# Kernel tuning notes

Measured on AMD Instinct MI355X. Metric: run time of the kernel, lower is better.

The kernel has to match this reference:

```python
import jax, jax.numpy as jnp
import numpy as np

B, N, D_IN, H1, H2, L, SEM_H = 256, 128, 1024, 512, 256, 64, 32


def _topo_sort(adj_np):
    # Faithful replica of the source DFS 'topological sort' (treats row entries as neighbors,
    # appends node after visiting them, then reverses). Runs on concrete numpy at setup time.
    n = adj_np.shape[0]
    visited = [False] * n
    order = []
    def dfs(u):
        visited[u] = True
        for v in np.nonzero(adj_np[u])[0]:
            if not visited[v]:
                dfs(v)
        order.append(u)
    for u in range(n):
        if not visited[u]:
            dfs(u)
    return np.array(order[::-1], dtype=np.int32)


def setup_inputs() -> dict:
    key = jax.random.key(0)
    ks = jax.random.split(key, 32)
    def w(k, shape, fan_in):
        return jax.random.normal(k, shape, jnp.float32) / np.float32(np.sqrt(fan_in))
    inp = {
        'x': jax.random.normal(ks[0], (B, N, D_IN), jnp.float32),
        'eps': jax.random.normal(ks[1], (B, N, L), jnp.float32),
        'adj_logits': jax.random.normal(ks[2], (N, N), jnp.float32),
        # encoder: D_IN -> H1 -> H2
        'enc_W1': w(ks[3], (H1, D_IN), D_IN), 'enc_b1': jnp.zeros((H1,), jnp.float32),
        'enc_W2': w(ks[4], (H2, H1), H1),     'enc_b2': jnp.zeros((H2,), jnp.float32),
        'mu_W': w(ks[5], (L, H2), H2),        'mu_b': jnp.zeros((L,), jnp.float32),
        'lv_W': w(ks[6], (L, H2), H2),        'lv_b': jnp.zeros((L,), jnp.float32),
        # decoder: L -> H2 -> H1 -> D_IN (reversed(hidden_dims), final Linear(hidden_dims[0], D_IN))
        'dec_W1': w(ks[7], (H2, L), L),       'dec_b1': jnp.zeros((H2,), jnp.float32),
        'dec_W2': w(ks[8], (H1, H2), H2),     'dec_b2': jnp.zeros((H1,), jnp.float32),
        'dec_W3': w(ks[9], (D_IN, H1), H1),   'dec_b3': jnp.zeros((D_IN,), jnp.float32),
        # per-node SEM MLPs, stacked: Linear(2L, 32) -> ReLU -> Linear(32, L)
        'sem_W1': w(ks[10], (N, SEM_H, 2 * L), 2 * L), 'sem_b1': jnp.zeros((N, SEM_H), jnp.float32),
        'sem_W2': w(ks[11], (N, L, SEM_H), SEM_H),     'sem_b2': jnp.zeros((N, L), jnp.float32),
    }
    # deterministic eval-mode adjacency -> concrete topo order
    mask = 1.0 - np.eye(N, dtype=np.float32)
    adj_np = (np.asarray(inp['adj_logits']) * mask) > 0
    inp['topo_order'] = jnp.asarray(_topo_sort(adj_np))
    return inp


def reference(x, eps, adj_logits, enc_W1, enc_b1, enc_W2, enc_b2, mu_W, mu_b, lv_W, lv_b,
              dec_W1, dec_b1, dec_W2, dec_b2, dec_W3, dec_b3, sem_W1, sem_b1, sem_W2, sem_b2,
              topo_order):
    f32 = x.dtype
    # --- adjacency (eval mode: hard threshold of masked logits) ---
    mask = 1.0 - jnp.eye(N, dtype=f32)
    adj = ((adj_logits * mask) > 0).astype(f32)  # [N, N], row i = parents of node i
    # --- encode ---
    h = jax.nn.relu(jnp.einsum('bnd,hd->bnh', x, enc_W1) + enc_b1)
    h = jax.nn.relu(jnp.einsum('bnd,hd->bnh', h, enc_W2) + enc_b2)
    mu = jnp.einsum('bnd,ld->bnl', h, mu_W) + mu_b
    logvar = jnp.einsum('bnd,ld->bnl', h, lv_W) + lv_b
    # --- reparameterize ---
    z = mu + eps * jnp.exp(0.5 * logvar)  # [B, N, L]
    # --- SEM: sequential scan over topological order ---
    def step(tz, node):
        adj_row = adj[node]                              # [N]
        cnt = jnp.maximum(adj_row.sum(), 1.0)
        agg = jnp.einsum('n,bnl->bl', adj_row, tz) / cnt  # mean over parents
        feat = jnp.concatenate([z[:, node], agg], axis=-1)  # [B, 2L]
        hh = jax.nn.relu(feat @ sem_W1[node].T + sem_b1[node])
        out = hh @ sem_W2[node].T + sem_b2[node]          # [B, L]
        return tz.at[:, node].set(out), None
    tz0 = jnp.zeros_like(z)
    z_t, _ = jax.lax.scan(step, tz0, topo_order)
    # --- decode ---
    d = jax.nn.relu(jnp.einsum('bnl,hl->bnh', z_t, dec_W1) + dec_b1)
    d = jax.nn.relu(jnp.einsum('bnl,hl->bnh', d, dec_W2) + dec_b2)
    recon_x = jnp.einsum('bnl,hl->bnh', d, dec_W3) + dec_b3
    # --- KL ---
    kl_div = -0.5 * jnp.sum(1.0 + logvar - mu * mu - jnp.exp(logvar))
    return recon_x, mu, logvar, adj, kl_div
```

## Files before the change

kernel.cpp:

```cpp
#include <hip/hip_runtime.h>
#include <cstdint>
#include <cstddef>

typedef unsigned short u16;
typedef __attribute__((ext_vector_type(8))) short short8;
typedef __attribute__((ext_vector_type(4))) float f32x4;

__device__ __forceinline__ u16 f2b(float f) {
  union { float f; uint32_t u; } v; v.f = f;
  uint32_t u = v.u;
  uint32_t r = (u + 0x7FFFu + ((u >> 16) & 1u)) >> 16;
  return (u16)r;
}

__device__ __forceinline__ void gload_lds16(const void* g, void* l) {
  __builtin_amdgcn_global_load_lds(
      (const __attribute__((address_space(1))) void*)g,
      (__attribute__((address_space(3))) void*)l, 16, 0, 0);
}
__device__ __forceinline__ void gload_lds4(const void* g, void* l) {
  __builtin_amdgcn_global_load_lds(
      (const __attribute__((address_space(1))) void*)g,
      (__attribute__((address_space(3))) void*)l, 4, 0, 0);
}

__global__ void prep_adj(const float* __restrict__ logits, const int* __restrict__ topo,
                         float* __restrict__ adj_out, int* __restrict__ parlist,
                         int* __restrict__ ecnt, float* __restrict__ rcnt,
                         const float* __restrict__ mu_b, const float* __restrict__ lv_b,
                         float* __restrict__ mbias) {
  __shared__ int pos[128];
  int i = threadIdx.x;
  pos[topo[i]] = i;
  __syncthreads();
  int mypos = pos[i];
  int c_all = 0, c_eff = 0;
  for (int j = 0; j < 128; ++j) {
    float v = (i != j && logits[i * 128 + j] > 0.0f) ? 1.0f : 0.0f;
    adj_out[i * 128 + j] = v;
    if (v != 0.0f) {
      c_all++;
      if (pos[j] < mypos) parlist[i * 128 + c_eff++] = j;
    }
  }
  while (c_eff & 15) parlist[i * 128 + c_eff++] = 128;
  ecnt[i] = c_eff;
  rcnt[i] = 1.0f / fmaxf((float)c_all, 1.0f);
  mbias[i] = (i < 64) ? mu_b[i] : lv_b[i - 64];
}

__global__ void prep_semT(const float* __restrict__ W1, const float* __restrict__ W2,
                          const float* __restrict__ b1, const float* __restrict__ b2,
                          float* __restrict__ W1T, float* __restrict__ W2T,
                          float* __restrict__ biasP) {
  int node = blockIdx.x, t = threadIdx.x;
  const float* w1 = W1 + node * 4096;
  float* o1 = W1T + node * 4096;
  for (int e = t; e < 4096; e += 256) { int j = e >> 7, k = e & 127; o1[k * 32 + j] = w1[e]; }
  const float* w2 = W2 + node * 2048;
  float* o2 = W2T + node * 2048;
  for (int e = t; e < 2048; e += 256) { int l = e >> 5, k = e & 31; o2[k * 64 + l] = w2[e]; }
  if (t < 128) {
    float v = 0.0f;
    if (t < 32) v = b1[node * 32 + t];
    else if (t < 96) v = b2[node * 64 + (t - 32)];
    biasP[node * 128 + t] = v;
  }
}

__global__ __launch_bounds__(256)
void cvt_weights(const float* __restrict__ e1, const float* __restrict__ e2,
                 const float* __restrict__ muw, const float* __restrict__ lvw,
                 const float* __restrict__ d1, const float* __restrict__ d2,
                 const float* __restrict__ d3, u16* __restrict__ dst) {
  int i = blockIdx.x * 256 + threadIdx.x;
  int stride = gridDim.x * 256;
  for (; i < 1359872; i += stride) {
    float v;
    if      (i < 524288) v = e1[i];
    else if (i < 655360) v = e2[i - 524288];
    else if (i < 671744) v = muw[i - 655360];
    else if (i < 688128) v = lvw[i - 671744];
    else if (i < 704512) v = d1[i - 688128];
    else if (i < 835584) v = d2[i - 704512];
    else                 v = d3[i - 835584];
    dst[i] = f2b(v);
  }
}

__global__ __launch_bounds__(256)
void cvt_f32_bf16(const float* __restrict__ src, u16* __restrict__ dst, size_t n4) {
  size_t i = (size_t)blockIdx.x * blockDim.x + threadIdx.x;
  size_t stride = (size_t)gridDim.x * blockDim.x;
  for (; i < n4; i += stride) {
    float4 v = ((const float4*)src)[i];
    ushort4 o;
    o.x = f2b(v.x); o.y = f2b(v.y); o.z = f2b(v.z); o.w = f2b(v.w);
    ((ushort4*)dst)[i] = o;
  }
}

template <int OUT_MODE, int RELU>
__global__ __launch_bounds__(256)
void gemm_bt(const u16* __restrict__ A, const u16* __restrict__ W,
             const float* __restrict__ bias, void* __restrict__ Cout,
             int M, int Ncols, int K, int gx) {
  __shared__ __align__(16) u16 As[128 * 64];
  __shared__ __align__(16) u16 Bs[128 * 64];
  const int tid = threadIdx.x;
  const int bid = blockIdx.x;
  const int xcd = bid & 7, w = bid >> 3;
  const int gy8 = (int)(gridDim.x >> 3) / gx;
  const int tile_n = w % gx;
  const int tile_m = xcd * gy8 + w / gx;
  const int wid = tid >> 6, lane = tid & 63;
  const int wm = (wid >> 1) * 64, wn = (wid & 1) * 64;
  const int lr = lane & 15, lg = lane >> 4;
  f32x4 acc[4][4] = {};
  const size_t arow0 = (size_t)tile_m * 128;
  const size_t brow0 = (size_t)tile_n * 128;

  for (int kt = 0; kt < K; kt += 64) {
#pragma unroll
    for (int is = 0; is < 4; ++is) {
      int e = is * 2048 + tid * 8;
      int r = e >> 6, c = e & 63;
      gload_lds16(A + (arow0 + r) * K + kt + c, &As[e]);
      gload_lds16(W + (brow0 + r) * K + kt + c, &Bs[e]);
    }
    __syncthreads();
#pragma unroll
    for (int kk = 0; kk < 64; kk += 32) {
      short8 av[4], bv[4];
#pragma unroll
      for (int m = 0; m < 4; ++m)
        av[m] = *(const short8*)&As[(wm + m * 16 + lr) * 64 + kk + lg * 8];
#pragma unroll
      for (int n = 0; n < 4; ++n)
        bv[n] = *(const short8*)&Bs[(wn + n * 16 + lr) * 64 + kk + lg * 8];
#pragma unroll
      for (int m = 0; m < 4; ++m)
#pragma unroll
        for (int n = 0; n < 4; ++n)
          acc[m][n] = __builtin_amdgcn_mfma_f32_16x16x32_bf16(av[m], bv[n], acc[m][n], 0, 0, 0);
    }
    __syncthreads();
  }
#pragma unroll
  for (int n = 0; n < 4; ++n) {
    int col = (int)brow0 + wn + n * 16 + lr;
    float bval = bias[col];
#pragma unroll
    for (int m = 0; m < 4; ++m) {
#pragma unroll
      for (int r = 0; r < 4; ++r) {
        int row = (int)arow0 + wm + m * 16 + lg * 4 + r;
        float v = acc[m][n][r] + bval;
        if (RELU) v = fmaxf(v, 0.0f);
        if (OUT_MODE == 1) ((u16*)Cout)[(size_t)row * Ncols + col] = f2b(v);
        else if (OUT_MODE == 0) ((float*)Cout)[(size_t)row * Ncols + col] = v;
        else {
          float* muo = (float*)Cout;
          float* lvo = muo + 2097152;
          if (col < 64) muo[(size_t)row * 64 + col] = v;
          else          lvo[(size_t)row * 64 + (col - 64)] = v;
        }
      }
    }
  }
}

__global__ __launch_bounds__(256)
void reparam_kernel(const float* __restrict__ mo, const float* __restrict__ lo,
                    const float* __restrict__ eps,
                    float* __restrict__ z, float* __restrict__ klpart) {
  int gid = blockIdx.x * 256 + threadIdx.x;
  float mu = mo[gid];
  float lv = lo[gid];
  float e = eps[gid];
  z[gid] = mu + e * expf(0.5f * lv);
  float kt = 1.0f + lv - mu * mu - expf(lv);
  for (int o = 32; o > 0; o >>= 1) kt += __shfl_down(kt, o);
  __shared__ float red[4];
  int lane = threadIdx.x & 63, w = threadIdx.x >> 6;
  if (lane == 0) red[w] = kt;
  __syncthreads();
  if (threadIdx.x == 0) klpart[blockIdx.x] = red[0] + red[1] + red[2] + red[3];
}

__global__ void kl_final(const float* __restrict__ klpart, float* __restrict__ out) {
  __shared__ float red[256];
  float s = 0.0f;
  for (int i = threadIdx.x; i < 8192; i += 256) s += klpart[i];
  red[threadIdx.x] = s;
  __syncthreads();
  for (int st = 128; st > 0; st >>= 1) {
    if (threadIdx.x < st) red[threadIdx.x] += red[threadIdx.x + st];
    __syncthreads();
  }
  if (threadIdx.x == 0) out[0] = -0.5f * red[0];
}

__device__ __forceinline__ void sem_pref(int wid, int lane, int nd, int bi, int b,
    const float* __restrict__ W1Tg, const float* __restrict__ W2Tg,
    const float* __restrict__ biasPg, const int* __restrict__ parlist,
    const float* __restrict__ z,
    float (*w1s)[4096], float (*w2s)[2048], int (*pls)[128],
    float (*zrs)[64], float (*bis)[128]) {
  const float* w1g = W1Tg + (size_t)nd * 4096 + wid * 1024 + lane * 4;
  float* w1d = &w1s[bi][wid * 1024 + lane * 4];
#pragma unroll
  for (int q = 0; q < 4; ++q) gload_lds16(w1g + q * 256, w1d + q * 256);
  if (wid >= 2) {
    int h = wid - 2;
    const float* w2g = W2Tg + (size_t)nd * 2048 + h * 1024 + lane * 4;
    float* w2d = &w2s[bi][h * 1024 + lane * 4];
#pragma unroll
    for (int q = 0; q < 4; ++q) gload_lds16(w2g + q * 256, w2d + q * 256);
  } else if (wid == 0) {
    gload_lds4(parlist + nd * 128 + lane, &pls[bi][lane]);
    gload_lds4(parlist + nd * 128 + 64 + lane, &pls[bi][64 + lane]);
  } else {
    gload_lds4(z + ((size_t)b * 128 + nd) * 64 + lane, &zrs[bi][lane]);
    gload_lds4(biasPg + nd * 128 + lane, &bis[bi][lane]);
    gload_lds4(biasPg + nd * 128 + 64 + lane, &bis[bi][64 + lane]);
  }
}

__global__ __launch_bounds__(256)
void sem_scan4(const float* __restrict__ z, u16* __restrict__ ztb,
               const float* __restrict__ W1Tg, const float* __restrict__ W2Tg,
               const float* __restrict__ biasPg,
               const int* __restrict__ parlist, const int* __restrict__ ecnt,
               const float* __restrict__ rcnt, const int* __restrict__ topo) {
  const int b = blockIdx.x, t = threadIdx.x;
  const int lane = t & 63, wid = t >> 6;
  __shared__ __align__(16) float tz[129 * 64];
  __shared__ __align__(16) float w1s[2][4096];
  __shared__ __align__(16) float w2s[2][2048];
  __shared__ __align__(16) int   pls[2][128];
  __shared__ __align__(16) float zrs[2][64];
  __shared__ __align__(16) float bis[2][128];
  __shared__ float feat[128];
  __shared__ float aggP[256];
  __shared__ float part1[128];
  __shared__ float part2[256];
  __shared__ float hhs[32];
  __shared__ int topoS[128];
  __shared__ int ecS[128];
  __shared__ float rcS[128];

  for (int i = t; i < 129 * 64; i += 256) tz[i] = 0.0f;
  if (t < 128) { topoS[t] = topo[t]; ecS[t] = ecnt[t]; rcS[t] = rcnt[t]; }
  __syncthreads();

  sem_pref(wid, lane, topoS[0], 0, b, W1Tg, W2Tg, biasPg, parlist, z,
           w1s, w2s, pls, zrs, bis);

  for (int s = 0; s < 128; ++s) {
    const int cur = s & 1;
    const int node = topoS[s];
    asm volatile("s_waitcnt vmcnt(0)" ::: "memory");
    __syncthreads();
    if (s + 1 < 128)
      sem_pref(wid, lane, topoS[s + 1], cur ^ 1, b, W1Tg, W2Tg, biasPg, parlist, z,
               w1s, w2s, pls, zrs, bis);

    const int pc = ecS[node];
    const int* pl = pls[cur];
    float ap = 0.0f;
    for (int i = wid * 16; i < pc; i += 64) {
      int4 p0 = *(const int4*)&pl[i];
      int4 p1 = *(const int4*)&pl[i + 4];
      int4 p2 = *(const int4*)&pl[i + 8];
      int4 p3 = *(const int4*)&pl[i + 12];
      ap += tz[p0.x * 64 + lane]; ap += tz[p0.y * 64 + lane];
      ap += tz[p0.z * 64 + lane]; ap += tz[p0.w * 64 + lane];
      ap += tz[p1.x * 64 + lane]; ap += tz[p1.y * 64 + lane];
      ap += tz[p1.z * 64 + lane]; ap += tz[p1.w * 64 + lane];
      ap += tz[p2.x * 64 + lane]; ap += tz[p2.y * 64 + lane];
      ap += tz[p2.z * 64 + lane]; ap += tz[p2.w * 64 + lane];
      ap += tz[p3.x * 64 + lane]; ap += tz[p3.y * 64 + lane];
      ap += tz[p3.z * 64 + lane]; ap += tz[p3.w * 64 + lane];
    }
    aggP[wid * 64 + lane] = ap;
    __syncthreads();
    if (t < 64) {
      float agg = (aggP[t] + aggP[64 + t] + aggP[128 + t] + aggP[192 + t]) * rcS[node];
      feat[t] = zrs[cur][t];
      feat[64 + t] = agg;
    }
    __syncthreads();

    {
      const int j = t & 31, sub = t >> 5;
      const float* w1 = &w1s[cur][sub * 512];
      float a = 0.0f;
#pragma unroll
      for (int kk = 0; kk < 16; ++kk)
        a = fmaf(w1[kk * 32 + j], feat[sub * 16 + kk], a);
      a += __shfl_xor(a, 32);
      if (lane < 32) part1[wid * 32 + j] = a;
    }
    __syncthreads();
    if (t < 32) {
      float hv = part1[t] + part1[32 + t] + part1[64 + t] + part1[96 + t] + bis[cur][t];
      hhs[t] = fmaxf(hv, 0.0f);
    }
    __syncthreads();

    {
      const float* w2 = &w2s[cur][wid * 512];
      float o = 0.0f;
#pragma unroll
      for (int kk = 0; kk < 8; ++kk)
        o = fmaf(w2[kk * 64 + lane], hhs[wid * 8 + kk], o);
      part2[wid * 64 + lane] = o;
    }
    __syncthreads();
    if (t < 64) {
      float ov = part2[t] + part2[64 + t] + part2[128 + t] + part2[192 + t] + bis[cur][32 + t];
      tz[node * 64 + t] = ov;
      ztb[((size_t)b * 128 + node) * 64 + t] = f2b(ov);
    }
  }
}

extern "C" void kernel_launch(void* const* d_in, const int* in_sizes, int n_in,
                              void* d_out, int out_size, void* d_ws, size_t ws_size,
                              hipStream_t stream) {
  const float* x          = (const float*)d_in[0];
  const float* eps        = (const float*)d_in[1];
  const float* adj_logits = (const float*)d_in[2];
  const float* enc_W1     = (const float*)d_in[3];
  const float* enc_b1     = (const float*)d_in[4];
  const float* enc_W2     = (const float*)d_in[5];
  const float* enc_b2     = (const float*)d_in[6];
  const float* mu_W       = (const float*)d_in[7];
  const float* mu_b       = (const float*)d_in[8];
  const float* lv_W       = (const float*)d_in[9];
  const float* lv_b       = (const float*)d_in[10];
  const float* dec_W1     = (const float*)d_in[11];
  const float* dec_b1     = (const float*)d_in[12];
  const float* dec_W2     = (const float*)d_in[13];
  const float* dec_b2     = (const float*)d_in[14];
  const float* dec_W3     = (const float*)d_in[15];
  const float* dec_b3     = (const float*)d_in[16];
  const float* sem_W1     = (const float*)d_in[17];
  const float* sem_b1     = (const float*)d_in[18];
  const float* sem_W2     = (const float*)d_in[19];
  const float* sem_b2     = (const float*)d_in[20];
  const int*   topo       = (const int*)d_in[21];

  float* out       = (float*)d_out;
  float* out_recon = out;
  float* out_mu    = out + 33554432;
  float* out_lv    = out + 35651584;
  float* out_adj   = out + 37748736;
  float* out_kl    = out + 37765120;

  char* ws = (char*)d_ws;
  u16*   xb      = (u16*)(ws + 0);
  u16*   d2b     = (u16*)(ws + 0);
  u16*   h1b     = (u16*)(ws + 67108864);
  u16*   d1b     = h1b;
  u16*   h2b     = (u16*)(ws + 100663296);
  float* zbuf    = (float*)(ws + 117440512);
  u16*   ztb     = (u16*)(ws + 125829120);
  u16*   wb      = (u16*)(ws + 130023424);
  float* W1T     = (float*)(ws + 132743168);
  float* W2T     = (float*)(ws + 134840320);
  float* biasP   = (float*)(ws + 135888896);
  int*   parlist = (int*)(ws + 135954432);
  int*   ecnt    = (int*)(ws + 136019968);
  float* rcnt    = (float*)(ws + 136020480);
  float* mbias   = (float*)(ws + 136020992);
  float* klp     = (float*)(ws + 136021504);

  u16* wE1 = wb;
  u16* wE2 = wb + 524288;
  u16* wML = wb + 655360;
  u16* wD1 = wb + 688128;
  u16* wD2 = wb + 704512;
  u16* wD3 = wb + 835584;

  prep_adj<<<1, 128, 0, stream>>>(adj_logits, topo, out_adj, parlist, ecnt, rcnt, mu_b, lv_b, mbias);
  prep_semT<<<128, 256, 0, stream>>>(sem_W1, sem_W2, sem_b1, sem_b2, W1T, W2T, biasP);
  cvt_weights<<<512, 256, 0, stream>>>(enc_W1, enc_W2, mu_W, lv_W, dec_W1, dec_W2, dec_W3, wb);
  cvt_f32_bf16<<<4096, 256, 0, stream>>>(x, xb, 8388608);

  dim3 blk(256);
  gemm_bt<1, 1><<<dim3(4 * 256), blk, 0, stream>>>(xb,  wE1, enc_b1, h1b,    32768, 512, 1024, 4);
  gemm_bt<1, 1><<<dim3(2 * 256), blk, 0, stream>>>(h1b, wE2, enc_b2, h2b,    32768, 256, 512, 2);
  gemm_bt<2, 0><<<dim3(1 * 256), blk, 0, stream>>>(h2b, wML, mbias,  out_mu, 32768, 128, 256, 1);

  reparam_kernel<<<8192, 256, 0, stream>>>(out_mu, out_lv, eps, zbuf, klp);
  kl_final<<<1, 256, 0, stream>>>(klp, out_kl);

  sem_scan4<<<256, 256, 0, stream>>>(zbuf, ztb, W1T, W2T, biasP, parlist, ecnt, rcnt, topo);

  gemm_bt<1, 1><<<dim3(2 * 256), blk, 0, stream>>>(ztb, wD1, dec_b1, d1b,       32768, 256, 64, 2);
  gemm_bt<1, 1><<<dim3(4 * 256), blk, 0, stream>>>(d1b, wD2, dec_b2, d2b,       32768, 512, 256, 4);
  gemm_bt<0, 0><<<dim3(8 * 256), blk, 0, stream>>>(d2b, wD3, dec_b3, out_recon, 32768, 1024, 512, 8);
}
```

Before: 715.1 us.

## Parallelize adjacency prep, swizzle SEM weights, cut scan barriers, vectorize reparam

prep_adj now runs one block per node and builds each parent list with ballot/popcount instead of a single-block serial loop. The SEM W1 weights are stored with an XOR swizzle, and the per-step matvecs are restructured to reduce with shuffles, which removes two barriers and the partial-sum buffers per scan step. The scan also waits on fewer outstanding loads for some waves, and reparam uses float4 loads with a quarter as many blocks. The aim is to shorten the latency-bound sequential scan; the risk is the changed vmcnt wait and the shuffle reduction indexing.

```diff
diff --git a/kernel.cpp b/kernel.cpp
--- a/kernel.cpp
+++ b/kernel.cpp
@@ -24,42 +24,58 @@
       (__attribute__((address_space(3))) void*)l, 4, 0, 0);
 }
 
-__global__ void prep_adj(const float* __restrict__ logits, const int* __restrict__ topo,
-                         float* __restrict__ adj_out, int* __restrict__ parlist,
-                         int* __restrict__ ecnt, float* __restrict__ rcnt,
-                         const float* __restrict__ mu_b, const float* __restrict__ lv_b,
-                         float* __restrict__ mbias) {
-  __shared__ int pos[128];
-  int i = threadIdx.x;
-  pos[topo[i]] = i;
+__global__ __launch_bounds__(64)
+void prep_adj(const float* __restrict__ logits, const int* __restrict__ topo,
+              float* __restrict__ adj_out, int* __restrict__ parlist,
+              int* __restrict__ ecnt, float* __restrict__ rcnt,
+              const float* __restrict__ mu_b, const float* __restrict__ lv_b,
+              float* __restrict__ mbias) {
+  __shared__ int pos_s[128];
+  const int i = blockIdx.x, lane = threadIdx.x;
+  pos_s[topo[lane]] = lane;
+  pos_s[topo[64 + lane]] = 64 + lane;
   __syncthreads();
-  int mypos = pos[i];
-  int c_all = 0, c_eff = 0;
-  for (int j = 0; j < 128; ++j) {
-    float v = (i != j && logits[i * 128 + j] > 0.0f) ? 1.0f : 0.0f;
-    adj_out[i * 128 + j] = v;
-    if (v != 0.0f) {
-      c_all++;
-      if (pos[j] < mypos) parlist[i * 128 + c_eff++] = j;
-    }
-  }
-  while (c_eff & 15) parlist[i * 128 + c_eff++] = 128;
-  ecnt[i] = c_eff;
-  rcnt[i] = 1.0f / fmaxf((float)c_all, 1.0f);
-  mbias[i] = (i < 64) ? mu_b[i] : lv_b[i - 64];
-}
-
-__global__ void prep_semT(const float* __restrict__ W1, const float* __restrict__ W2,
+  const int myp = pos_s[i];
+  bool edge0 = (i != lane) && (logits[i * 128 + lane] > 0.0f);
+  bool edge1 = (i != 64 + lane) && (logits[i * 128 + 64 + lane] > 0.0f);
+  adj_out[i * 128 + lane] = edge0 ? 1.0f : 0.0f;
+  adj_out[i * 128 + 64 + lane] = edge1 ? 1.0f : 0.0f;
+  bool par0 = edge0 && (pos_s[lane] < myp);
+  bool par1 = edge1 && (pos_s[64 + lane] < myp);
+  uint64_t m0 = __ballot(par0);
+  uint64_t m1 = __ballot(par1);
+  uint64_t below = (lane == 0) ? 0ull : ((~0ull) >> (64 - lane));
+  int c0 = __popcll(m0);
+  int c_eff = c0 + __popcll(m1);
+  if (par0) parlist[i * 128 + __popcll(m0 & below)] = lane;
+  if (par1) parlist[i * 128 + c0 + __popcll(m1 & below)] = 64 + lane;
+  int padded = (c_eff + 15) & ~15;
+  if (lane < padded - c_eff) parlist[i * 128 + c_eff + lane] = 128;
+  int c_all = __popcll(__ballot(edge0)) + __popcll(__ballot(edge1));
+  if (lane == 0) {
+    ecnt[i] = padded;
+    rcnt[i] = 1.0f / fmaxf((float)c_all, 1.0f);
+    mbias[i] = (i < 64) ? mu_b[i] : lv_b[i - 64];
+  }
+}
+
+__global__ void prep_semS(const float* __restrict__ W1, const float* __restrict__ W2,
                           const float* __restrict__ b1, const float* __restrict__ b2,
-                          float* __restrict__ W1T, float* __restrict__ W2T,
+                          float* __restrict__ W1S, float* __restrict__ W2T,
                           float* __restrict__ biasP) {
   int node = blockIdx.x, t = threadIdx.x;
   const float* w1 = W1 + node * 4096;
-  float* o1 = W1T + node * 4096;
-  for (int e = t; e < 4096; e += 256) { int j = e >> 7, k = e & 127; o1[k * 32 + j] = w1[e]; }
+  float* o1 = W1S + node * 4096;
+  for (int d = t; d < 4096; d += 256) {
+    int k = d >> 5, jx = d & 31, j = jx ^ ((k & 7) << 2);
+    o1[d] = w1[j * 128 + k];
+  }
   const float* w2 = W2 + node * 2048;
   float* o2 = W2T + node * 2048;
-  for (int e = t; e < 2048; e += 256) { int l = e >> 5, k = e & 31; o2[k * 64 + l] = w2[e]; }
+  for (int d = t; d < 2048; d += 256) {
+    int k = d >> 6, l = d & 63;
+    o2[d] = w2[l * 32 + k];
+  }
   if (t < 128) {
     float v = 0.0f;
     if (t < 32) v = b1[node * 32 + t];
@@ -175,11 +191,18 @@
                     const float* __restrict__ eps,
                     float* __restrict__ z, float* __restrict__ klpart) {
   int gid = blockIdx.x * 256 + threadIdx.x;
-  float mu = mo[gid];
-  float lv = lo[gid];
-  float e = eps[gid];
-  z[gid] = mu + e * expf(0.5f * lv);
-  float kt = 1.0f + lv - mu * mu - expf(lv);
+  float4 mu4 = ((const float4*)mo)[gid];
+  float4 lv4 = ((const float4*)lo)[gid];
+  float4 e4  = ((const float4*)eps)[gid];
+  float4 z4;
+  z4.x = mu4.x + e4.x * expf(0.5f * lv4.x);
+  z4.y = mu4.y + e4.y * expf(0.5f * lv4.y);
+  z4.z = mu4.z + e4.z * expf(0.5f * lv4.z);
+  z4.w = mu4.w + e4.w * expf(0.5f * lv4.w);
+  ((float4*)z)[gid] = z4;
+  float kt = 4.0f + lv4.x + lv4.y + lv4.z + lv4.w
+           - mu4.x * mu4.x - mu4.y * mu4.y - mu4.z * mu4.z - mu4.w * mu4.w
+           - expf(lv4.x) - expf(lv4.y) - expf(lv4.z) - expf(lv4.w);
   for (int o = 32; o > 0; o >>= 1) kt += __shfl_down(kt, o);
   __shared__ float red[4];
   int lane = threadIdx.x & 63, w = threadIdx.x >> 6;
@@ -191,7 +214,7 @@
 __global__ void kl_final(const float* __restrict__ klpart, float* __restrict__ out) {
   __shared__ float red[256];
   float s = 0.0f;
-  for (int i = threadIdx.x; i < 8192; i += 256) s += klpart[i];
+  for (int i = threadIdx.x; i < 2048; i += 256) s += klpart[i];
   red[threadIdx.x] = s;
   __syncthreads();
   for (int st = 128; st > 0; st >>= 1) {
@@ -202,12 +225,12 @@
 }
 
 __device__ __forceinline__ void sem_pref(int wid, int lane, int nd, int bi, int b,
-    const float* __restrict__ W1Tg, const float* __restrict__ W2Tg,
+    const float* __restrict__ W1Sg, const float* __restrict__ W2Tg,
     const float* __restrict__ biasPg, const int* __restrict__ parlist,
     const float* __restrict__ z,
     float (*w1s)[4096], float (*w2s)[2048], int (*pls)[128],
     float (*zrs)[64], float (*bis)[128]) {
-  const float* w1g = W1Tg + (size_t)nd * 4096 + wid * 1024 + lane * 4;
+  const float* w1g = W1Sg + (size_t)nd * 4096 + wid * 1024 + lane * 4;
   float* w1d = &w1s[bi][wid * 1024 + lane * 4];
 #pragma unroll
   for (int q = 0; q < 4; ++q) gload_lds16(w1g + q * 256, w1d + q * 256);
@@ -229,7 +252,7 @@
 
 __global__ __launch_bounds__(256)
 void sem_scan4(const float* __restrict__ z, u16* __restrict__ ztb,
-               const float* __restrict__ W1Tg, const float* __restrict__ W2Tg,
+               const float* __restrict__ W1Sg, const float* __restrict__ W2Tg,
                const float* __restrict__ biasPg,
                const int* __restrict__ parlist, const int* __restrict__ ecnt,
                const float* __restrict__ rcnt, const int* __restrict__ topo) {
@@ -243,8 +266,6 @@
   __shared__ __align__(16) float bis[2][128];
   __shared__ float feat[128];
   __shared__ float aggP[256];
-  __shared__ float part1[128];
-  __shared__ float part2[256];
   __shared__ float hhs[32];
   __shared__ int topoS[128];
   __shared__ int ecS[128];
@@ -254,16 +275,18 @@
   if (t < 128) { topoS[t] = topo[t]; ecS[t] = ecnt[t]; rcS[t] = rcnt[t]; }
   __syncthreads();
 
-  sem_pref(wid, lane, topoS[0], 0, b, W1Tg, W2Tg, biasPg, parlist, z,
+  sem_pref(wid, lane, topoS[0], 0, b, W1Sg, W2Tg, biasPg, parlist, z,
            w1s, w2s, pls, zrs, bis);
 
   for (int s = 0; s < 128; ++s) {
     const int cur = s & 1;
     const int node = topoS[s];
-    asm volatile("s_waitcnt vmcnt(0)" ::: "memory");
+    if (s > 0 && wid < 2) asm volatile("s_waitcnt vmcnt(1)" ::: "memory");
+    else                  asm volatile("s_waitcnt vmcnt(0)" ::: "memory");
+    __builtin_amdgcn_sched_barrier(0);
     __syncthreads();
     if (s + 1 < 128)
-      sem_pref(wid, lane, topoS[s + 1], cur ^ 1, b, W1Tg, W2Tg, biasPg, parlist, z,
+      sem_pref(wid, lane, topoS[s + 1], cur ^ 1, b, W1Sg, W2Tg, biasPg, parlist, z,
                w1s, w2s, pls, zrs, bis);
 
     const int pc = ecS[node];
@@ -286,42 +309,41 @@
     aggP[wid * 64 + lane] = ap;
     __syncthreads();
     if (t < 64) {
-      float agg = (aggP[t] + aggP[64 + t] + aggP[128 + t] + aggP[192 + t]) * rcS[node];
       feat[t] = zrs[cur][t];
-      feat[64 + t] = agg;
-    }
-    __syncthreads();
-
+      feat[64 + t] = (aggP[t] + aggP[64 + t] + aggP[128 + t] + aggP[192 + t]) * rcS[node];
+    }
+    __syncthreads();
     {
-      const int j = t & 31, sub = t >> 5;
-      const float* w1 = &w1s[cur][sub * 512];
+      const int sub = lane & 7, j = wid * 8 + (lane >> 3);
+      const float* w1 = w1s[cur];
+      const int jx = j ^ (sub << 2);
       float a = 0.0f;
 #pragma unroll
-      for (int kk = 0; kk < 16; ++kk)
-        a = fmaf(w1[kk * 32 + j], feat[sub * 16 + kk], a);
-      a += __shfl_xor(a, 32);
-      if (lane < 32) part1[wid * 32 + j] = a;
-    }
-    __syncthreads();
-    if (t < 32) {
-      float hv = part1[t] + part1[32 + t] + part1[64 + t] + part1[96 + t] + bis[cur][t];
-      hhs[t] = fmaxf(hv, 0.0f);
-    }
-    __syncthreads();
-
-    {
-      const float* w2 = &w2s[cur][wid * 512];
+      for (int i = 0; i < 16; ++i) {
+        int k = sub + 8 * i;
+        a = fmaf(w1[k * 32 + jx], feat[k], a);
+      }
+      a += __shfl_xor(a, 1);
+      a += __shfl_xor(a, 2);
+      a += __shfl_xor(a, 4);
+      if (sub == 0) hhs[j] = fmaxf(a + bis[cur][j], 0.0f);
+    }
+    __syncthreads();
+    if (t < 128) {
+      const int ss = t & 1, l = t >> 1;
+      const float* w2 = w2s[cur];
       float o = 0.0f;
 #pragma unroll
-      for (int kk = 0; kk < 8; ++kk)
-        o = fmaf(w2[kk * 64 + lane], hhs[wid * 8 + kk], o);
-      part2[wid * 64 + lane] = o;
-    }
-    __syncthreads();
-    if (t < 64) {
-      float ov = part2[t] + part2[64 + t] + part2[128 + t] + part2[192 + t] + bis[cur][32 + t];
-      tz[node * 64 + t] = ov;
-      ztb[((size_t)b * 128 + node) * 64 + t] = f2b(ov);
+      for (int i = 0; i < 16; ++i) {
+        int k = ss + 2 * i;
+        o = fmaf(w2[k * 64 + l], hhs[k], o);
+      }
+      o += __shfl_xor(o, 1);
+      if (ss == 0) {
+        float ov = o + bis[cur][32 + l];
+        tz[node * 64 + l] = ov;
+        ztb[((size_t)b * 128 + node) * 64 + l] = f2b(ov);
+      }
     }
   }
 }
@@ -368,7 +390,7 @@
   float* zbuf    = (float*)(ws + 117440512);
   u16*   ztb     = (u16*)(ws + 125829120);
   u16*   wb      = (u16*)(ws + 130023424);
-  float* W1T     = (float*)(ws + 132743168);
+  float* W1S     = (float*)(ws + 132743168);
   float* W2T     = (float*)(ws + 134840320);
   float* biasP   = (float*)(ws + 135888896);
   int*   parlist = (int*)(ws + 135954432);
@@ -384,8 +406,8 @@
   u16* wD2 = wb + 704512;
   u16* wD3 = wb + 835584;
 
-  prep_adj<<<1, 128, 0, stream>>>(adj_logits, topo, out_adj, parlist, ecnt, rcnt, mu_b, lv_b, mbias);
-  prep_semT<<<128, 256, 0, stream>>>(sem_W1, sem_W2, sem_b1, sem_b2, W1T, W2T, biasP);
+  prep_adj<<<128, 64, 0, stream>>>(adj_logits, topo, out_adj, parlist, ecnt, rcnt, mu_b, lv_b, mbias);
+  prep_semS<<<128, 256, 0, stream>>>(sem_W1, sem_W2, sem_b1, sem_b2, W1S, W2T, biasP);
   cvt_weights<<<512, 256, 0, stream>>>(enc_W1, enc_W2, mu_W, lv_W, dec_W1, dec_W2, dec_W3, wb);
   cvt_f32_bf16<<<4096, 256, 0, stream>>>(x, xb, 8388608);
 
@@ -394,10 +416,10 @@
   gemm_bt<1, 1><<<dim3(2 * 256), blk, 0, stream>>>(h1b, wE2, enc_b2, h2b,    32768, 256, 512, 2);
   gemm_bt<2, 0><<<dim3(1 * 256), blk, 0, stream>>>(h2b, wML, mbias,  out_mu, 32768, 128, 256, 1);
 
-  reparam_kernel<<<8192, 256, 0, stream>>>(out_mu, out_lv, eps, zbuf, klp);
+  reparam_kernel<<<2048, 256, 0, stream>>>(out_mu, out_lv, eps, zbuf, klp);
   kl_final<<<1, 256, 0, stream>>>(klp, out_kl);
 
-  sem_scan4<<<256, 256, 0, stream>>>(zbuf, ztb, W1T, W2T, biasP, parlist, ecnt, rcnt, topo);
+  sem_scan4<<<256, 256, 0, stream>>>(zbuf, ztb, W1S, W2T, biasP, parlist, ecnt, rcnt, topo);
 
   gemm_bt<1, 1><<<dim3(2 * 256), blk, 0, stream>>>(ztb, wD1, dec_b1, d1b,       32768, 256, 64, 2);
   gemm_bt<1, 1><<<dim3(4 * 256), blk, 0, stream>>>(d1b, wD2, dec_b2, d2b,       32768, 512, 256, 4);
```

Measured after the change: 683.4 us. 1.05x faster.
